# Optimization experiments

Hardware: AMD Instinct MI355X
Metric: run time of the kernel (lower is better)

Reference implementation:

```python
import jax, jax.numpy as jnp
import numpy as np
import hashlib

B, L, D, STEPS, VOCAB = 4, 8192, 2048, 8, 50257


def _sha256_c(tid: int):
    # Same hashing as FractalEmbedding._token_to_c_batch
    h = hashlib.sha256(str(int(tid)).encode()).hexdigest()
    real = int(h[:16], 16) / 2**64 - 0.5
    imag = int(h[16:32], 16) / 2**64 - 0.5
    return (real * 2.0, imag * 2.0)


def setup_inputs() -> dict:
    key = jax.random.key(0)
    k1, k2 = jax.random.split(key)
    token_ids = jax.random.randint(k1, (B, L), 0, VOCAB, dtype=jnp.int64)
    # sha256 is host-side, non-differentiable integer hashing: precompute the
    # per-token Julia constant c (faithful to _token_to_c_batch). Hash only the
    # unique ids, then gather.
    ids = np.asarray(token_ids)
    uniq, inv = np.unique(ids, return_inverse=True)
    cs_u = np.array([_sha256_c(t) for t in uniq], dtype=np.float32)  # [U,2]
    cs = jnp.asarray(cs_u[inv].reshape(B, L, 2))                      # [B,L,2]
    # nn.Linear(2*steps, embed_dim, bias=False) weight: [D, 2*steps]
    W = jax.random.normal(k2, (D, 2 * STEPS), dtype=jnp.float32) / np.sqrt(2 * STEPS)
    scale = jnp.ones((), dtype=jnp.float32)
    return {"token_ids": token_ids, "cs": cs, "W": W, "scale": scale}


def reference(token_ids, cs, W, scale):
    # Julia iteration z <- z^2 + c starting from z=0, recording (zr, zi)
    # interleaved at every step -> feats [B,L,2*steps].
    steps = W.shape[1] // 2
    cr, ci = cs[..., 0], cs[..., 1]
    zr = jnp.zeros_like(cr)
    zi = jnp.zeros_like(ci)
    vals = []
    for _ in range(steps):  # steps=8, tiny static loop
        zr, zi = zr * zr - zi * zi + cr, 2.0 * zr * zi + ci
        vals.append(zr)
        vals.append(zi)
    feats = jnp.stack(vals, axis=-1)  # [B,L,2*steps], interleaved re/im
    # out = proj(feats) * scale, proj has no bias
    return jnp.einsum('blf,df->bld', feats, W) * scale
```

## Files before the change

### kernel.cpp

```cpp
#include <hip/hip_runtime.h>


#define STEPS 8
#define KF 16
#define DDIM 2048
#define BLOCK 256
#define DPT 4
#define D_PER_BLK (BLOCK * DPT)
#define D_BLOCKS (DDIM / D_PER_BLK)
#define ROWS_PER_BLK 32

static_assert(D_BLOCKS == 2, "rblk shift assumes 2 d-blocks");

typedef float f32x2 __attribute__((ext_vector_type(2)));
typedef float f32x4 __attribute__((ext_vector_type(4)));

__global__ __launch_bounds__(BLOCK) void fractal_embed_kernel(
    const float* __restrict__ cs,
    const float* __restrict__ W,
    const float* __restrict__ scale,
    float* __restrict__ out)
{
    const int tid  = threadIdx.x;
    const int dblk = blockIdx.x & (D_BLOCKS - 1);
    const int rblk = blockIdx.x >> 1;
    const int d0   = dblk * D_PER_BLK + tid * DPT;
    const int row0 = rblk * ROWS_PER_BLK;

    __shared__ float s_cs[2 * ROWS_PER_BLK];
    if (tid < 2 * ROWS_PER_BLK)
        s_cs[tid] = cs[(size_t)row0 * 2 + tid];

    f32x2 w2[DPT][KF / 2];
#pragma unroll
    for (int r = 0; r < DPT; ++r) {
        const f32x2* wp = reinterpret_cast<const f32x2*>(W + (size_t)(d0 + r) * KF);
#pragma unroll
        for (int q = 0; q < KF / 2; ++q) w2[r][q] = wp[q];
    }
    const float s = scale[0];

    __syncthreads();

#pragma unroll 2
    for (int rr = 0; rr < ROWS_PER_BLK; ++rr) {
        const int row = row0 + rr;
        const float cr = s_cs[2 * rr];
        const float ci = s_cs[2 * rr + 1];

        f32x2 f2[STEPS];
        float zr = 0.0f, zi = 0.0f;
#pragma unroll
        for (int st = 0; st < STEPS; ++st) {
            const float nzr = fmaf(zr, zr, fmaf(-zi, zi, cr));
            const float nzi = fmaf(zr + zr, zi, ci);
            zr = nzr; zi = nzi;
            f2[st].x = zr;
            f2[st].y = zi;
        }

        f32x4 o;
#pragma unroll
        for (int r = 0; r < DPT; ++r) {
            f32x2 a2 = {0.0f, 0.0f};
#pragma unroll
            for (int q = 0; q < KF / 2; ++q)
                a2 = __builtin_elementwise_fma(f2[q], w2[r][q], a2);
            o[r] = (a2.x + a2.y) * s;
        }

        reinterpret_cast<f32x4*>(out + (size_t)row * DDIM + d0)[0] = o;
    }
}

extern "C" void kernel_launch(void* const* d_in, const int* in_sizes, int n_in,
                              void* d_out, int out_size, void* d_ws, size_t ws_size,
                              hipStream_t stream) {
    const float* cs    = (const float*)d_in[1];
    const float* W     = (const float*)d_in[2];
    const float* scale = (const float*)d_in[3];
    float* out         = (float*)d_out;

    const int M = in_sizes[0];
    const int grid = D_BLOCKS * (M / ROWS_PER_BLK);
    fractal_embed_kernel<<<grid, BLOCK, 0, stream>>>(cs, W, scale, out);
}
```

Before: 58.76 us.

## Compute projection with split-bf16 MFMA instead of scalar FP32 FMAs

Measured after the change: 62.17 us. 1.06x slower.

```diff
diff --git a/kernel.cpp b/kernel.cpp
--- a/kernel.cpp
+++ b/kernel.cpp
@@ -5,71 +5,108 @@
 #define KF 16
 #define DDIM 2048
 #define BLOCK 256
-#define DPT 4
-#define D_PER_BLK (BLOCK * DPT)
-#define D_BLOCKS (DDIM / D_PER_BLK)
-#define ROWS_PER_BLK 32
+#define WAVES 4
+#define NCT 8
+#define COLS_PER_WAVE (NCT * 16)
+#define CGROUPS (DDIM / COLS_PER_WAVE)
+#define RT_PER_WAVE 4
+#define ROWS_PER_BLOCK (WAVES * RT_PER_WAVE * 16)
 
-static_assert(D_BLOCKS == 2, "rblk shift assumes 2 d-blocks");
+static_assert(CGROUPS == 16, "blockIdx decomposition assumes 16 col groups");
 
-typedef float f32x2 __attribute__((ext_vector_type(2)));
-typedef float f32x4 __attribute__((ext_vector_type(4)));
+typedef float f32x2  __attribute__((ext_vector_type(2)));
+typedef float f32x4  __attribute__((ext_vector_type(4)));
+typedef short bf16x8 __attribute__((ext_vector_type(8)));
 
-__global__ __launch_bounds__(BLOCK) void fractal_embed_kernel(
+static __device__ inline unsigned short bf16_rne(float x) {
+    unsigned u = __float_as_uint(x);
+    u += 0x7FFFu + ((u >> 16) & 1u);
+    return (unsigned short)(u >> 16);
+}
+static __device__ inline float bf16_f32(unsigned short h) {
+    return __uint_as_float(((unsigned)h) << 16);
+}
+
+__global__ __launch_bounds__(BLOCK) void fractal_embed_mfma(
     const float* __restrict__ cs,
     const float* __restrict__ W,
     const float* __restrict__ scale,
     float* __restrict__ out)
 {
     const int tid  = threadIdx.x;
-    const int dblk = blockIdx.x & (D_BLOCKS - 1);
-    const int rblk = blockIdx.x >> 1;
-    const int d0   = dblk * D_PER_BLK + tid * DPT;
-    const int row0 = rblk * ROWS_PER_BLK;
+    const int lane = tid & 63;
+    const int wv   = tid >> 6;
+    const int r15  = lane & 15;
+    const int g    = lane >> 4;
 
-    __shared__ float s_cs[2 * ROWS_PER_BLK];
-    if (tid < 2 * ROWS_PER_BLK)
-        s_cs[tid] = cs[(size_t)row0 * 2 + tid];
+    const int cg    = blockIdx.x & (CGROUPS - 1);
+    const int rg    = blockIdx.x >> 4;
+    const int dwave = cg * COLS_PER_WAVE;
+    const int rt0   = (rg * WAVES + wv) * RT_PER_WAVE;
 
-    f32x2 w2[DPT][KF / 2];
+    f32x2 cpre[RT_PER_WAVE];
 #pragma unroll
-    for (int r = 0; r < DPT; ++r) {
-        const f32x2* wp = reinterpret_cast<const f32x2*>(W + (size_t)(d0 + r) * KF);
-#pragma unroll
-        for (int q = 0; q < KF / 2; ++q) w2[r][q] = wp[q];
-    }
+    for (int t = 0; t < RT_PER_WAVE; ++t)
+        cpre[t] = reinterpret_cast<const f32x2*>(cs)[(rt0 + t) * 16 + r15];
+
     const float s = scale[0];
 
-    __syncthreads();
+    bf16x8 wh[NCT], wl[NCT];
+#pragma unroll
+    for (int ct = 0; ct < NCT; ++ct) {
+        const int d = dwave + ct * 16 + r15;
+        f32x4 a0 = {0.f, 0.f, 0.f, 0.f}, a1 = {0.f, 0.f, 0.f, 0.f};
+        if (g < 2) {
+            const f32x4* wp = reinterpret_cast<const f32x4*>(W + (size_t)d * KF + g * 8);
+            a0 = wp[0];
+            a1 = wp[1];
+        }
+        float v[8] = {a0.x * s, a0.y * s, a0.z * s, a0.w * s,
+                      a1.x * s, a1.y * s, a1.z * s, a1.w * s};
+#pragma unroll
+        for (int e = 0; e < 8; ++e) {
+            const unsigned short hh = bf16_rne(v[e]);
+            const float lo = v[e] - bf16_f32(hh);
+            wh[ct][e] = (short)hh;
+            wl[ct][e] = (short)bf16_rne(lo);
+        }
+    }
 
-#pragma unroll 2
-    for (int rr = 0; rr < ROWS_PER_BLK; ++rr) {
-        const int row = row0 + rr;
-        const float cr = s_cs[2 * rr];
-        const float ci = s_cs[2 * rr + 1];
+#pragma unroll
+    for (int t = 0; t < RT_PER_WAVE; ++t) {
+        const int rowbase = (rt0 + t) * 16;
+        const float cr = cpre[t].x, ci = cpre[t].y;
 
-        f32x2 f2[STEPS];
-        float zr = 0.0f, zi = 0.0f;
+        float fk[2 * STEPS];
+        float zr = 0.f, zi = 0.f;
 #pragma unroll
         for (int st = 0; st < STEPS; ++st) {
             const float nzr = fmaf(zr, zr, fmaf(-zi, zi, cr));
             const float nzi = fmaf(zr + zr, zi, ci);
             zr = nzr; zi = nzi;
-            f2[st].x = zr;
-            f2[st].y = zi;
+            fk[2 * st] = zr;
+            fk[2 * st + 1] = zi;
         }
 
-        f32x4 o;
+        bf16x8 bh, bl;
 #pragma unroll
-        for (int r = 0; r < DPT; ++r) {
-            f32x2 a2 = {0.0f, 0.0f};
-#pragma unroll
-            for (int q = 0; q < KF / 2; ++q)
-                a2 = __builtin_elementwise_fma(f2[q], w2[r][q], a2);
-            o[r] = (a2.x + a2.y) * s;
+        for (int e = 0; e < 8; ++e) {
+            const float v = (g == 0) ? fk[e] : ((g == 1) ? fk[8 + e] : 0.0f);
+            const unsigned short hh = bf16_rne(v);
+            const float lo = v - bf16_f32(hh);
+            bh[e] = (short)hh;
+            bl[e] = (short)bf16_rne(lo);
         }
 
-        reinterpret_cast<f32x4*>(out + (size_t)row * DDIM + d0)[0] = o;
+        float* op = out + (size_t)(rowbase + r15) * DDIM + dwave + g * 4;
+#pragma unroll
+        for (int ct = 0; ct < NCT; ++ct) {
+            f32x4 acc = {0.f, 0.f, 0.f, 0.f};
+            acc = __builtin_amdgcn_mfma_f32_16x16x32_bf16(wh[ct], bh, acc, 0, 0, 0);
+            acc = __builtin_amdgcn_mfma_f32_16x16x32_bf16(wh[ct], bl, acc, 0, 0, 0);
+            acc = __builtin_amdgcn_mfma_f32_16x16x32_bf16(wl[ct], bh, acc, 0, 0, 0);
+            reinterpret_cast<f32x4*>(op + ct * 16)[0] = acc;
+        }
     }
 }
 
@@ -82,6 +119,7 @@
     float* out         = (float*)d_out;
 
     const int M = in_sizes[0];
-    const int grid = D_BLOCKS * (M / ROWS_PER_BLK);
-    fractal_embed_kernel<<<grid, BLOCK, 0, stream>>>(cs, W, scale, out);
+    const int rowgroups = M / ROWS_PER_BLOCK;
+    const int grid = CGROUPS * rowgroups;
+    fractal_embed_mfma<<<grid, BLOCK, 0, stream>>>(cs, W, scale, out);
 }
```

## Cover full embedding row per block and fold scale into weights

Applied to the files above, without the earlier changes.

After: 57.00 us. -3.0%, faster.

```diff
diff --git a/kernel.cpp b/kernel.cpp
--- a/kernel.cpp
+++ b/kernel.cpp
@@ -5,41 +5,41 @@
 #define KF 16
 #define DDIM 2048
 #define BLOCK 256
-#define DPT 4
-#define D_PER_BLK (BLOCK * DPT)
-#define D_BLOCKS (DDIM / D_PER_BLK)
+#define CPT 8
 #define ROWS_PER_BLK 32
-
-static_assert(D_BLOCKS == 2, "rblk shift assumes 2 d-blocks");
 
 typedef float f32x2 __attribute__((ext_vector_type(2)));
 typedef float f32x4 __attribute__((ext_vector_type(4)));
 
-__global__ __launch_bounds__(BLOCK) void fractal_embed_kernel(
+__global__ __launch_bounds__(BLOCK, 2) void fractal_embed_kernel(
     const float* __restrict__ cs,
     const float* __restrict__ W,
     const float* __restrict__ scale,
     float* __restrict__ out)
 {
     const int tid  = threadIdx.x;
-    const int dblk = blockIdx.x & (D_BLOCKS - 1);
-    const int rblk = blockIdx.x >> 1;
-    const int d0   = dblk * D_PER_BLK + tid * DPT;
-    const int row0 = rblk * ROWS_PER_BLK;
+    const int row0 = blockIdx.x * ROWS_PER_BLK;
+    const int ca   = tid * 4;
+    const int cb   = 1024 + tid * 4;
 
     __shared__ float s_cs[2 * ROWS_PER_BLK];
     if (tid < 2 * ROWS_PER_BLK)
         s_cs[tid] = cs[(size_t)row0 * 2 + tid];
 
-    f32x2 w2[DPT][KF / 2];
-#pragma unroll
-    for (int r = 0; r < DPT; ++r) {
-        const f32x2* wp = reinterpret_cast<const f32x2*>(W + (size_t)(d0 + r) * KF);
-#pragma unroll
-        for (int q = 0; q < KF / 2; ++q) w2[r][q] = wp[q];
-    }
     const float s = scale[0];
 
+    f32x2 w2[CPT][KF / 2];
+#pragma unroll
+    for (int r = 0; r < CPT; ++r) {
+        const int d = (r < 4) ? (ca + r) : (cb + (r - 4));
+        const f32x2* wp = reinterpret_cast<const f32x2*>(W + (size_t)d * KF);
+#pragma unroll
+        for (int q = 0; q < KF / 2; ++q) {
+            f32x2 v = wp[q];
+            v.x *= s; v.y *= s;
+            w2[r][q] = v;
+        }
+    }
     __syncthreads();
 
 #pragma unroll 2
@@ -59,17 +59,21 @@
             f2[st].y = zi;
         }
 
-        f32x4 o;
+        f32x4 oa, ob;
 #pragma unroll
-        for (int r = 0; r < DPT; ++r) {
+        for (int r = 0; r < CPT; ++r) {
             f32x2 a2 = {0.0f, 0.0f};
 #pragma unroll
             for (int q = 0; q < KF / 2; ++q)
                 a2 = __builtin_elementwise_fma(f2[q], w2[r][q], a2);
-            o[r] = (a2.x + a2.y) * s;
+            const float v = a2.x + a2.y;
+            if (r < 4) oa[r] = v;
+            else       ob[r - 4] = v;
         }
 
-        reinterpret_cast<f32x4*>(out + (size_t)row * DDIM + d0)[0] = o;
+        float* rowp = out + (size_t)row * DDIM;
+        reinterpret_cast<f32x4*>(rowp + ca)[0] = oa;
+        reinterpret_cast<f32x4*>(rowp + cb)[0] = ob;
     }
 }
 
@@ -82,6 +86,6 @@
     float* out         = (float*)d_out;
 
     const int M = in_sizes[0];
-    const int grid = D_BLOCKS * (M / ROWS_PER_BLK);
+    const int grid = M / ROWS_PER_BLK;
     fractal_embed_kernel<<<grid, BLOCK, 0, stream>>>(cs, W, scale, out);
 }
```
